# Performance work log

Hardware: AMD Instinct MI355X
Metric: run time of the kernel (lower is better)

Reference implementation:

```python
import jax, jax.numpy as jnp
import numpy as np

B, T, N, D, W = 8, 24, 1024, 64, 2
EPS = 1e-5


def setup_inputs() -> dict:
    key = jax.random.key(0)
    ks = jax.random.split(key, 6)
    s = 1.0 / np.sqrt(D)
    x = jax.random.normal(ks[0], (B, T, N, D), dtype=jnp.float32)
    W1 = jax.random.normal(ks[1], (D, D), dtype=jnp.float32) * s
    b1 = jax.random.normal(ks[2], (D,), dtype=jnp.float32) * s
    W2 = jax.random.normal(ks[3], (D, D), dtype=jnp.float32) * s
    b2 = jax.random.normal(ks[4], (D,), dtype=jnp.float32) * s
    gamma = jnp.ones((D,), dtype=jnp.float32)
    beta = jnp.zeros((D,), dtype=jnp.float32)
    # expanded_adj: [N, N*W] = [I | I | ...], then row-normalized (norm_adj ~ D^-1 A)
    adj = jnp.tile(jnp.eye(N, dtype=jnp.float32), (1, W))
    adj = adj / jnp.clip(adj.sum(axis=1, keepdims=True), 1.0, None)
    return {"x": x, "W1": W1, "b1": b1, "W2": W2, "b2": b2,
            "gamma": gamma, "beta": beta, "adj": adj}


def reference(x, W1, b1, W2, b2, gamma, beta, adj):
    Bx, Tx, Nx, Dx = x.shape
    win = adj.shape[1] // Nx
    feat = jnp.pad(x, ((0, 0), (win - 1, 0), (0, 0), (0, 0)))
    g = jnp.stack([feat[:, i:i + Tx] for i in range(win)], axis=2)
    g = g.reshape(Bx, Tx, win * Nx, Dx)
    h1 = jnp.einsum('btmd,ed->btme', g, W1) + b1
    h2 = jnp.einsum('btmd,ed->btme', g, W2) + b2
    a1 = jnp.einsum('nm,btme->btne', adj, h1)  # [B,T,N,D]
    a2 = jnp.einsum('nm,btme->btne', adj, h2)
    full = jax.nn.relu(a1 * a2) + a1
    z = full + x
    mu = z.mean(axis=-1, keepdims=True)
    var = z.var(axis=-1, keepdims=True)
    return (z - mu) * jax.lax.rsqrt(var + EPS) * gamma + beta
```

## Files before the change

### kernel.cpp

```cpp
#include <hip/hip_runtime.h>

#define BB 8
#define TT 24
#define NN 1024
#define DD 64
#define CHAIN 4

typedef float  f32x4  __attribute__((ext_vector_type(4)));
typedef __bf16 bf16x8 __attribute__((ext_vector_type(8)));

#define LOADC(dst, ptr) do {                         \
    dst[0] = *(const f32x4*)((ptr) + q8);            \
    dst[1] = *(const f32x4*)((ptr) + q8 + 4);        \
    dst[2] = *(const f32x4*)((ptr) + 32 + q8);       \
    dst[3] = *(const f32x4*)((ptr) + 36 + q8);       \
} while (0)

#define STEP(K, PRV, CUR, DO_PREF, C0K) do {                                       \
    const size_t off = off0 + (size_t)(K) * (NN * DD);                             \
    const float* xr = x + off;                                                     \
            \
    f32x4 xe[4];                                                                   \
    _Pragma("unroll")                                                              \
    for (int et = 0; et < 4; ++et)                                                 \
        xe[et] = *(const f32x4*)(xr + et * 16 + e4);                               \
          \
    bf16x8 X0, X1;                                                                 \
    _Pragma("unroll")                                                              \
    for (int j = 0; j < 4; ++j) {                                                  \
        X0[j]     = (__bf16)((C0K) * PRV[0][j] + c1 * CUR[0][j]);                  \
        X0[j + 4] = (__bf16)((C0K) * PRV[1][j] + c1 * CUR[1][j]);                  \
        X1[j]     = (__bf16)((C0K) * PRV[2][j] + c1 * CUR[2][j]);                  \
        X1[j + 4] = (__bf16)((C0K) * PRV[3][j] + c1 * CUR[3][j]);                  \
    }                                                                              \
          \
    __builtin_amdgcn_sched_barrier(0);                                             \
                 \
    if (DO_PREF) { LOADC(PRV, xr + NN * DD); }                                     \
                        \
    f32x4 acc1[4], acc2[4];                                                        \
    _Pragma("unroll")                                                              \
    for (int et = 0; et < 4; ++et) {                                               \
        acc1[et] = (f32x4){0.f, 0.f, 0.f, 0.f};                                    \
        acc2[et] = (f32x4){0.f, 0.f, 0.f, 0.f};                                    \
    }                                                                              \
    _Pragma("unroll")                                                              \
    for (int et = 0; et < 4; ++et) {                                               \
        const bf16x8 w10 = wlds[et * 2 + 0][lane];                                 \
        const bf16x8 w11 = wlds[et * 2 + 1][lane];                                 \
        const bf16x8 w20 = wlds[8 + et * 2 + 0][lane];                             \
        const bf16x8 w21 = wlds[8 + et * 2 + 1][lane];                             \
        acc1[et] = __builtin_amdgcn_mfma_f32_16x16x32_bf16(w10, X0, acc1[et], 0, 0, 0); \
        acc1[et] = __builtin_amdgcn_mfma_f32_16x16x32_bf16(w11, X1, acc1[et], 0, 0, 0); \
        acc2[et] = __builtin_amdgcn_mfma_f32_16x16x32_bf16(w20, X0, acc2[et], 0, 0, 0); \
        acc2[et] = __builtin_amdgcn_mfma_f32_16x16x32_bf16(w21, X1, acc2[et], 0, 0, 0); \
    }                                                                              \
       \
    float s = 0.f, s2 = 0.f;                                                       \
    _Pragma("unroll")                                                              \
    for (int et = 0; et < 4; ++et) {                                               \
        const f32x4 b1v = plds[0][et * 4 + quad];                                  \
        const f32x4 b2v = plds[1][et * 4 + quad];                                  \
        _Pragma("unroll")                                                          \
        for (int r = 0; r < 4; ++r) {                                              \
            const float A1v = acc1[et][r] + cb * b1v[r];                           \
            const float A2v = acc2[et][r] + cb * b2v[r];                           \
            const float p   = A1v * A2v;                                           \
            const float full = (p > 0.f ? p : 0.f) + A1v;                          \
            const float zz = full + xe[et][r];                                     \
            acc1[et][r] = zz;                                                      \
            s  += zz;                                                              \
            s2 += zz * zz;                                                         \
        }                                                                          \
    }                                                                              \
    s  += __shfl_xor(s, 16, 64);                                                   \
    s2 += __shfl_xor(s2, 16, 64);                                                  \
    s  += __shfl_xor(s, 32, 64);                                                   \
    s2 += __shfl_xor(s2, 32, 64);                                                  \
    const float mu  = s * (1.f / 64.f);                                            \
    const float var = s2 * (1.f / 64.f) - mu * mu;                                 \
    const float rs  = rsqrtf(var + 1e-5f);                                         \
    float* orow = out + off;                                                       \
    _Pragma("unroll")                                                              \
    for (int et = 0; et < 4; ++et) {                                               \
        const f32x4 gvv = plds[2][et * 4 + quad];                                  \
        const f32x4 bev = plds[3][et * 4 + quad];                                  \
        f32x4 o;                                                                   \
        _Pragma("unroll")                                                          \
        for (int r = 0; r < 4; ++r)                                                \
            o[r] = (acc1[et][r] - mu) * rs * gvv[r] + bev[r];                      \
        *(f32x4*)(orow + et * 16 + e4) = o;                                        \
    }                                                                              \
} while (0)

__global__ __launch_bounds__(256) void stgcn_kernel(
    const float* __restrict__ x,
    const float* __restrict__ W1,
    const float* __restrict__ b1,
    const float* __restrict__ W2,
    const float* __restrict__ b2,
    const float* __restrict__ gamma,
    const float* __restrict__ beta,
    const float* __restrict__ adj,
    float* __restrict__ out)
{
    const int tid  = threadIdx.x;
    const int lane = tid & 63;
    const int wv   = tid >> 6;
    const int m16  = lane & 15;
    const int quad = lane >> 4;
    const int e4   = quad * 4;
    const int q8   = quad * 8;

    __shared__ bf16x8 wlds[16][64];
    __shared__ f32x4  plds[4][16];

    for (int s = tid; s < 16 * 64; s += 256) {
        const int g  = s >> 6, l = s & 63;
        const int mat = g >> 3, et = (g >> 1) & 3, ks = g & 1;
        const int ms = l & 15, qs = l >> 4;
        const float* src = (mat ? W2 : W1) + (et * 16 + ms) * DD + ks * 32 + qs * 8;
        const f32x4 a  = *(const f32x4*)(src);
        const f32x4 bb = *(const f32x4*)(src + 4);
        bf16x8 f;
#pragma unroll
        for (int j = 0; j < 4; ++j) { f[j] = (__bf16)a[j]; f[j + 4] = (__bf16)bb[j]; }
        wlds[g][l] = f;
    }
    if (tid < 64) {
        const int arr = tid >> 4, j = tid & 15;
        const float* src = (arr == 0) ? b1 : (arr == 1) ? b2 : (arr == 2) ? gamma : beta;
        plds[arr][j] = *(const f32x4*)(src + j * 4);
    }
    __syncthreads();

    const int wid = blockIdx.x * 4 + wv;
    const int nt  = wid & 63;
    const int tg  = (wid >> 6) % 6;
    const int b   = wid / 384;
    const int t0  = tg * CHAIN;

    const int n = nt * 16 + m16;
    const float c0 = adj[(size_t)n * (NN * 2) + n];
    const float c1 = adj[(size_t)n * (NN * 2) + NN + n];
    const float cb = c0 + c1;
    const float c00 = (t0 > 0) ? c0 : 0.f;

    const size_t off0 = ((size_t)(b * TT + t0) * NN + nt * 16 + m16) * DD;

    f32x4 bufA[4], bufB[4];
    LOADC(bufB, x + off0);
    if (t0 > 0) {
        LOADC(bufA, x + off0 - NN * DD);
    } else {
        bufA[0] = bufA[1] = bufA[2] = bufA[3] = (f32x4){0.f, 0.f, 0.f, 0.f};
    }

    STEP(0, bufA, bufB, 1, c00);
    STEP(1, bufB, bufA, 1, c0);
    STEP(2, bufA, bufB, 1, c0);
    STEP(3, bufB, bufA, 0, c0);
}

extern "C" void kernel_launch(void* const* d_in, const int* in_sizes, int n_in,
                              void* d_out, int out_size, void* d_ws, size_t ws_size,
                              hipStream_t stream) {
    const float* x     = (const float*)d_in[0];
    const float* W1    = (const float*)d_in[1];
    const float* b1    = (const float*)d_in[2];
    const float* W2    = (const float*)d_in[3];
    const float* b2    = (const float*)d_in[4];
    const float* gamma = (const float*)d_in[5];
    const float* beta  = (const float*)d_in[6];
    const float* adj   = (const float*)d_in[7];
    float* out = (float*)d_out;

    dim3 grid(768), block(256);
    hipLaunchKernelGGL(stgcn_kernel, grid, block, 0, stream,
                       x, W1, b1, W2, b2, gamma, beta, adj, out);
}
```

Before: 123.7 us.

## Stage x tiles through LDS with async global_load_lds double buffering

Replaces per-lane global loads of x rows with asynchronous global-to-LDS copies into a per-wave double buffer, using an XOR swizzle to avoid bank conflicts. Both the current and previous timestep tiles and the residual term are then read from LDS instead of issuing separate global loads. Waits are managed with explicit vmcnt counts, overlapping the next timestep's load with compute. This adds 32KB of LDS per block, which may lower occupancy, and the hand-counted waits are fragile because output stores also count toward vmcnt.

```diff
diff --git a/kernel.cpp b/kernel.cpp
--- a/kernel.cpp
+++ b/kernel.cpp
@@ -4,94 +4,17 @@
 #define TT 24
 #define NN 1024
 #define DD 64
-#define CHAIN 4
 
 typedef float  f32x4  __attribute__((ext_vector_type(4)));
 typedef __bf16 bf16x8 __attribute__((ext_vector_type(8)));
 
-#define LOADC(dst, ptr) do {                         \
-    dst[0] = *(const f32x4*)((ptr) + q8);            \
-    dst[1] = *(const f32x4*)((ptr) + q8 + 4);        \
-    dst[2] = *(const f32x4*)((ptr) + 32 + q8);       \
-    dst[3] = *(const f32x4*)((ptr) + 36 + q8);       \
-} while (0)
+__device__ __forceinline__ void gload16(const void* g, void* l) {
+    __builtin_amdgcn_global_load_lds(
+        (const __attribute__((address_space(1))) void*)g,
+        (__attribute__((address_space(3)))       void*)l, 16, 0, 0);
+}
 
-#define STEP(K, PRV, CUR, DO_PREF, C0K) do {                                       \
-    const size_t off = off0 + (size_t)(K) * (NN * DD);                             \
-    const float* xr = x + off;                                                     \
-            \
-    f32x4 xe[4];                                                                   \
-    _Pragma("unroll")                                                              \
-    for (int et = 0; et < 4; ++et)                                                 \
-        xe[et] = *(const f32x4*)(xr + et * 16 + e4);                               \
-          \
-    bf16x8 X0, X1;                                                                 \
-    _Pragma("unroll")                                                              \
-    for (int j = 0; j < 4; ++j) {                                                  \
-        X0[j]     = (__bf16)((C0K) * PRV[0][j] + c1 * CUR[0][j]);                  \
-        X0[j + 4] = (__bf16)((C0K) * PRV[1][j] + c1 * CUR[1][j]);                  \
-        X1[j]     = (__bf16)((C0K) * PRV[2][j] + c1 * CUR[2][j]);                  \
-        X1[j + 4] = (__bf16)((C0K) * PRV[3][j] + c1 * CUR[3][j]);                  \
-    }                                                                              \
-          \
-    __builtin_amdgcn_sched_barrier(0);                                             \
-                 \
-    if (DO_PREF) { LOADC(PRV, xr + NN * DD); }                                     \
-                        \
-    f32x4 acc1[4], acc2[4];                                                        \
-    _Pragma("unroll")                                                              \
-    for (int et = 0; et < 4; ++et) {                                               \
-        acc1[et] = (f32x4){0.f, 0.f, 0.f, 0.f};                                    \
-        acc2[et] = (f32x4){0.f, 0.f, 0.f, 0.f};                                    \
-    }                                                                              \
-    _Pragma("unroll")                                                              \
-    for (int et = 0; et < 4; ++et) {                                               \
-        const bf16x8 w10 = wlds[et * 2 + 0][lane];                                 \
-        const bf16x8 w11 = wlds[et * 2 + 1][lane];                                 \
-        const bf16x8 w20 = wlds[8 + et * 2 + 0][lane];                             \
-        const bf16x8 w21 = wlds[8 + et * 2 + 1][lane];                             \
-        acc1[et] = __builtin_amdgcn_mfma_f32_16x16x32_bf16(w10, X0, acc1[et], 0, 0, 0); \
-        acc1[et] = __builtin_amdgcn_mfma_f32_16x16x32_bf16(w11, X1, acc1[et], 0, 0, 0); \
-        acc2[et] = __builtin_amdgcn_mfma_f32_16x16x32_bf16(w20, X0, acc2[et], 0, 0, 0); \
-        acc2[et] = __builtin_amdgcn_mfma_f32_16x16x32_bf16(w21, X1, acc2[et], 0, 0, 0); \
-    }                                                                              \
-       \
-    float s = 0.f, s2 = 0.f;                                                       \
-    _Pragma("unroll")                                                              \
-    for (int et = 0; et < 4; ++et) {                                               \
-        const f32x4 b1v = plds[0][et * 4 + quad];                                  \
-        const f32x4 b2v = plds[1][et * 4 + quad];                                  \
-        _Pragma("unroll")                                                          \
-        for (int r = 0; r < 4; ++r) {                                              \
-            const float A1v = acc1[et][r] + cb * b1v[r];                           \
-            const float A2v = acc2[et][r] + cb * b2v[r];                           \
-            const float p   = A1v * A2v;                                           \
-            const float full = (p > 0.f ? p : 0.f) + A1v;                          \
-            const float zz = full + xe[et][r];                                     \
-            acc1[et][r] = zz;                                                      \
-            s  += zz;                                                              \
-            s2 += zz * zz;                                                         \
-        }                                                                          \
-    }                                                                              \
-    s  += __shfl_xor(s, 16, 64);                                                   \
-    s2 += __shfl_xor(s2, 16, 64);                                                  \
-    s  += __shfl_xor(s, 32, 64);                                                   \
-    s2 += __shfl_xor(s2, 32, 64);                                                  \
-    const float mu  = s * (1.f / 64.f);                                            \
-    const float var = s2 * (1.f / 64.f) - mu * mu;                                 \
-    const float rs  = rsqrtf(var + 1e-5f);                                         \
-    float* orow = out + off;                                                       \
-    _Pragma("unroll")                                                              \
-    for (int et = 0; et < 4; ++et) {                                               \
-        const f32x4 gvv = plds[2][et * 4 + quad];                                  \
-        const f32x4 bev = plds[3][et * 4 + quad];                                  \
-        f32x4 o;                                                                   \
-        _Pragma("unroll")                                                          \
-        for (int r = 0; r < 4; ++r)                                                \
-            o[r] = (acc1[et][r] - mu) * rs * gvv[r] + bev[r];                      \
-        *(f32x4*)(orow + et * 16 + e4) = o;                                        \
-    }                                                                              \
-} while (0)
+#define WAITV(n) asm volatile("s_waitcnt vmcnt(" #n ")" ::: "memory")
 
 __global__ __launch_bounds__(256) void stgcn_kernel(
     const float* __restrict__ x,
@@ -110,9 +33,9 @@
     const int m16  = lane & 15;
     const int quad = lane >> 4;
     const int e4   = quad * 4;
-    const int q8   = quad * 8;
 
     __shared__ bf16x8 wlds[16][64];
+    __shared__ __align__(16) float xbuf[4][2][1024];
     __shared__ f32x4  plds[4][16];
 
     for (int s = tid; s < 16 * 64; s += 256) {
@@ -138,7 +61,7 @@
     const int nt  = wid & 63;
     const int tg  = (wid >> 6) % 6;
     const int b   = wid / 384;
-    const int t0  = tg * CHAIN;
+    const int t0  = tg * 4;
 
     const int n = nt * 16 + m16;
     const float c0 = adj[(size_t)n * (NN * 2) + n];
@@ -146,20 +69,114 @@
     const float cb = c0 + c1;
     const float c00 = (t0 > 0) ? c0 : 0.f;
 
-    const size_t off0 = ((size_t)(b * TT + t0) * NN + nt * 16 + m16) * DD;
+    char* const lb0 = (char*)&xbuf[wv][0][0];
+    char* const lb1 = (char*)&xbuf[wv][1][0];
+    auto stage = [&](int s, int t) {
+        const char* gb = (const char*)(x + ((size_t)(b * TT + t) * NN + nt * 16) * DD);
+        char* lb = s ? lb1 : lb0;
+#pragma unroll
+        for (int i = 0; i < 4; ++i) {
+            const int D = i * 1024 + lane * 16;
+            const int S = D ^ (((D >> 8) & 7) << 4);
+            gload16(gb + S, lb + D);
+        }
+    };
 
-    f32x4 bufA[4], bufB[4];
-    LOADC(bufB, x + off0);
-    if (t0 > 0) {
-        LOADC(bufA, x + off0 - NN * DD);
-    } else {
-        bufA[0] = bufA[1] = bufA[2] = bufA[3] = (f32x4){0.f, 0.f, 0.f, 0.f};
-    }
+    const int RB  = m16 * 256;
+    const int SW  = (m16 & 7) << 4;
+    const int q32 = quad * 32;
 
-    STEP(0, bufA, bufB, 1, c00);
-    STEP(1, bufB, bufA, 1, c0);
-    STEP(2, bufA, bufB, 1, c0);
-    STEP(3, bufB, bufA, 0, c0);
+    stage(0, (t0 > 0) ? t0 - 1 : t0);
+    stage(1, t0);
+    WAITV(4);
+    __builtin_amdgcn_sched_barrier(0);
+    f32x4 pA[4], cB[4], cA[4];
+    pA[0] = *(const f32x4*)(lb0 + ((RB + q32      ) ^ SW));
+    pA[1] = *(const f32x4*)(lb0 + ((RB + q32 + 16 ) ^ SW));
+    pA[2] = *(const f32x4*)(lb0 + ((RB + 128 + q32) ^ SW));
+    pA[3] = *(const f32x4*)(lb0 + ((RB + 144 + q32) ^ SW));
+
+#define STEPK(K, PRV, CUR, RBUF, WAITN, DO_STAGE, C0K) do {                        \
+    WAITV(WAITN);                                                                  \
+    __builtin_amdgcn_sched_barrier(0);                                             \
+    if (DO_STAGE) stage((K) & 1, t0 + (K) + 1);                                    \
+    __builtin_amdgcn_sched_barrier(0);                                             \
+    const char* rb = RBUF;                                                         \
+    CUR[0] = *(const f32x4*)(rb + ((RB + q32      ) ^ SW));                        \
+    CUR[1] = *(const f32x4*)(rb + ((RB + q32 + 16 ) ^ SW));                        \
+    CUR[2] = *(const f32x4*)(rb + ((RB + 128 + q32) ^ SW));                        \
+    CUR[3] = *(const f32x4*)(rb + ((RB + 144 + q32) ^ SW));                        \
+    f32x4 xe[4];                                                                   \
+    _Pragma("unroll")                                                              \
+    for (int et = 0; et < 4; ++et)                                                 \
+        xe[et] = *(const f32x4*)(rb + ((RB + et * 64 + quad * 16) ^ SW));          \
+    bf16x8 X0, X1;                                                                 \
+    _Pragma("unroll")                                                              \
+    for (int j = 0; j < 4; ++j) {                                                  \
+        X0[j]     = (__bf16)((C0K) * PRV[0][j] + c1 * CUR[0][j]);                  \
+        X0[j + 4] = (__bf16)((C0K) * PRV[1][j] + c1 * CUR[1][j]);                  \
+        X1[j]     = (__bf16)((C0K) * PRV[2][j] + c1 * CUR[2][j]);                  \
+        X1[j + 4] = (__bf16)((C0K) * PRV[3][j] + c1 * CUR[3][j]);                  \
+    }                                                                              \
+    f32x4 acc1[4], acc2[4];                                                        \
+    _Pragma("unroll")                                                              \
+    for (int et = 0; et < 4; ++et) {                                               \
+        acc1[et] = (f32x4){0.f, 0.f, 0.f, 0.f};                                    \
+        acc2[et] = (f32x4){0.f, 0.f, 0.f, 0.f};                                    \
+    }                                                                              \
+    _Pragma("unroll")                                                              \
+    for (int et = 0; et < 4; ++et) {                                               \
+        const bf16x8 w10 = wlds[et * 2 + 0][lane];                                 \
+        const bf16x8 w11 = wlds[et * 2 + 1][lane];                                 \
+        const bf16x8 w20 = wlds[8 + et * 2 + 0][lane];                             \
+        const bf16x8 w21 = wlds[8 + et * 2 + 1][lane];                             \
+        acc1[et] = __builtin_amdgcn_mfma_f32_16x16x32_bf16(w10, X0, acc1[et], 0, 0, 0); \
+        acc1[et] = __builtin_amdgcn_mfma_f32_16x16x32_bf16(w11, X1, acc1[et], 0, 0, 0); \
+        acc2[et] = __builtin_amdgcn_mfma_f32_16x16x32_bf16(w20, X0, acc2[et], 0, 0, 0); \
+        acc2[et] = __builtin_amdgcn_mfma_f32_16x16x32_bf16(w21, X1, acc2[et], 0, 0, 0); \
+    }                                                                              \
+    float s = 0.f, s2 = 0.f;                                                       \
+    _Pragma("unroll")                                                              \
+    for (int et = 0; et < 4; ++et) {                                               \
+        const f32x4 b1v = plds[0][et * 4 + quad];                                  \
+        const f32x4 b2v = plds[1][et * 4 + quad];                                  \
+        _Pragma("unroll")                                                          \
+        for (int r = 0; r < 4; ++r) {                                              \
+            const float A1v = acc1[et][r] + cb * b1v[r];                           \
+            const float A2v = acc2[et][r] + cb * b2v[r];                           \
+            const float p   = A1v * A2v;                                           \
+            const float full = (p > 0.f ? p : 0.f) + A1v;                          \
+            const float zz = full + xe[et][r];                                     \
+            acc1[et][r] = zz;                                                      \
+            s  += zz;                                                              \
+            s2 += zz * zz;                                                         \
+        }                                                                          \
+    }                                                                              \
+    s  += __shfl_xor(s, 16, 64);                                                   \
+    s2 += __shfl_xor(s2, 16, 64);                                                  \
+    s  += __shfl_xor(s, 32, 64);                                                   \
+    s2 += __shfl_xor(s2, 32, 64);                                                  \
+    const float mu  = s * (1.f / 64.f);                                            \
+    const float var = s2 * (1.f / 64.f) - mu * mu;                                 \
+    const float rs  = rsqrtf(var + 1e-5f);                                         \
+    float* orow = out + ((size_t)(b * TT + t0 + (K)) * NN + nt * 16 + m16) * DD;   \
+    _Pragma("unroll")                                                              \
+    for (int et = 0; et < 4; ++et) {                                               \
+        const f32x4 gvv = plds[2][et * 4 + quad];                                  \
+        const f32x4 bev = plds[3][et * 4 + quad];                                  \
+        f32x4 o;                                                                   \
+        _Pragma("unroll")                                                          \
+        for (int r = 0; r < 4; ++r)                                                \
+            o[r] = (acc1[et][r] - mu) * rs * gvv[r] + bev[r];                      \
+        *(f32x4*)(orow + et * 16 + e4) = o;                                        \
+    }                                                                              \
+} while (0)
+
+    STEPK(0, pA, cB, lb1, 0, 1, c00);
+    STEPK(1, cB, cA, lb0, 4, 1, c0);
+    STEPK(2, cA, pA, lb1, 4, 1, c0);
+    STEPK(3, pA, cB, lb0, 4, 0, c0);
+#undef STEPK
 }
 
 extern "C" void kernel_launch(void* const* d_in, const int* in_sizes, int n_in,
```

New measurement: 120.2 us. 1.03x faster.
